# Optimization experiments

Measured on AMD Instinct MI355X. Metric: run time of the kernel, lower is better.

The kernel has to match this reference:

```python
import jax, jax.numpy as jnp
import numpy as np

B, L, D, H, NB = 8, 256, 128, 4, 2
HD = D // H
N_ITEMS, TIME_SPAN = 50000, 256
EPS = 1e-8
NEG = -(2.0 ** 32) + 1.0  # torch uses -2**32+1 padding value


def _ln(x, g, b):
    m = jnp.mean(x, -1, keepdims=True)
    v = jnp.mean((x - m) ** 2, -1, keepdims=True)
    return (x - m) / jnp.sqrt(v + EPS) * g + b


def setup_inputs() -> dict:
    ks = iter(jax.random.split(jax.random.key(0), 40))

    def nrm(shape, s=0.02):
        return jax.random.normal(next(ks), shape, jnp.float32) * s

    inp = {
        "user_ids": jax.random.randint(next(ks), (B,), 0, 1000),
        "log_seqs": jax.random.randint(next(ks), (B, L), 0, N_ITEMS + 1),
        "time_matrices": jax.random.randint(next(ks), (B, L, L), 0, TIME_SPAN + 1),
        "pos_seqs": jax.random.randint(next(ks), (B, L), 1, N_ITEMS + 1),
        "neg_seqs": jax.random.randint(next(ks), (B, L), 1, N_ITEMS + 1),
    }
    inp["item_emb"] = nrm((N_ITEMS + 1, D)).at[0].set(0.0)  # padding_idx=0
    inp["posK_emb"] = nrm((L, D))
    inp["posV_emb"] = nrm((L, D))
    inp["timeK_emb"] = nrm((TIME_SPAN + 1, D))
    inp["timeV_emb"] = nrm((TIME_SPAN + 1, D))
    inp["ln1_g"] = jnp.ones((NB, D)); inp["ln1_b"] = jnp.zeros((NB, D))
    inp["Wq"] = nrm((NB, D, D)); inp["bq"] = jnp.zeros((NB, D))
    inp["Wk"] = nrm((NB, D, D)); inp["bk"] = jnp.zeros((NB, D))
    inp["Wv"] = nrm((NB, D, D)); inp["bv"] = jnp.zeros((NB, D))
    inp["ln2_g"] = jnp.ones((NB, D)); inp["ln2_b"] = jnp.zeros((NB, D))
    inp["W1"] = nrm((NB, D, D)); inp["b1"] = jnp.zeros((NB, D))
    inp["W2"] = nrm((NB, D, D)); inp["b2"] = jnp.zeros((NB, D))
    inp["lnf_g"] = jnp.ones((D,)); inp["lnf_b"] = jnp.zeros((D,))
    return inp


def reference(user_ids, log_seqs, time_matrices, pos_seqs, neg_seqs,
              item_emb, posK_emb, posV_emb, timeK_emb, timeV_emb,
              ln1_g, ln1_b, Wq, bq, Wk, bk, Wv, bv, ln2_g, ln2_b,
              W1, b1, W2, b2, lnf_g, lnf_b):
    # dropout layers are identity in eval mode
    seqs = item_emb[log_seqs] * jnp.sqrt(jnp.float32(D))          # [B,L,D]
    tK = timeK_emb[time_matrices].reshape(B, L, L, H, HD)          # [B,Lq,Lk,H,hd]
    tV = timeV_emb[time_matrices].reshape(B, L, L, H, HD)
    pad = log_seqs == 0                                            # [B,L]
    seqs = seqs * (~pad)[..., None]
    causal = jnp.triu(jnp.ones((L, L), bool), 1)                   # ~tril -> masked
    # time_mask masks by QUERY position (matches torch unsqueeze(-1).expand)
    mask = pad[:, None, :, None] | causal[None, None]              # [B,1,Lq,Lk]
    posKh = posK_emb.reshape(L, H, HD)
    posVh = posV_emb.reshape(L, H, HD)
    for i in range(NB):
        q_in = _ln(seqs, ln1_g[i], ln1_b[i])
        Qh = (q_in @ Wq[i] + bq[i]).reshape(B, L, H, HD).transpose(0, 2, 1, 3)
        Kh = (seqs @ Wk[i] + bk[i]).reshape(B, L, H, HD).transpose(0, 2, 1, 3)
        Vh = (seqs @ Wv[i] + bv[i]).reshape(B, L, H, HD).transpose(0, 2, 1, 3)
        scores = jnp.einsum("bhqd,bhkd->bhqk", Qh, Kh)
        scores = scores + jnp.einsum("bhqd,khd->bhqk", Qh, posKh)
        scores = scores + jnp.einsum("bqkhd,bhqd->bhqk", tK, Qh)
        scores = scores / jnp.sqrt(jnp.float32(HD))
        scores = jnp.where(mask, NEG, scores)
        A = jax.nn.softmax(scores, axis=-1)                        # [B,H,Lq,Lk]
        out = jnp.einsum("bhqk,bhkd->bhqd", A, Vh)
        out = out + jnp.einsum("bhqk,khd->bhqd", A, posVh)
        out = out + jnp.einsum("bhqk,bqkhd->bhqd", A, tV)
        out = out.transpose(0, 2, 1, 3).reshape(B, L, D)
        seqs = q_in + out                                          # residual on Q
        seqs = _ln(seqs, ln2_g[i], ln2_b[i])
        h = jax.nn.relu(seqs @ W1[i] + b1[i])                      # conv1d k=1 == linear
        seqs = seqs + (h @ W2[i] + b2[i])
        seqs = seqs * (~pad)[..., None]
    feats = _ln(seqs, lnf_g, lnf_b)
    pos_logits = jnp.sum(feats * item_emb[pos_seqs], -1)           # [B,L]
    neg_logits = jnp.sum(feats * item_emb[neg_seqs], -1)
    return (pos_logits, neg_logits)
```

## Files before the change

kernel.cpp:

```cpp
#include <hip/hip_runtime.h>
#include <hip/hip_bf16.h>

#define L_ 256
#define H_ 4
#define ROWS 2048
#define NEGV (-4294967295.0f)

typedef unsigned short us16;

__device__ __forceinline__ float us2f(us16 u){ return __uint_as_float(((unsigned)u)<<16); }
__device__ __forceinline__ us16 f2us(float f){ __hip_bfloat16 h=__float2bfloat16(f); return *(us16*)&h; }

struct KArgs {
    const int *log_seqs, *tmat, *pos_seqs, *neg_seqs;
    const float *item_emb, *posK, *posV, *timeK, *timeV;
    const float *ln1g, *ln1b, *bq, *bk, *bv, *ln2g, *ln2b, *b1, *b2, *lnfg, *lnfb;
    const float *Wq, *Wk, *Wv, *W1, *W2;
    float *qin0, *qin1, *out;
    us16 *wsW, *tmK, *tmV, *Qb0, *Kb0, *Vb0, *Qb1, *Kb1, *Vb1;
};

__device__ __forceinline__ void stage_w(const us16* __restrict__ Wg, us16* sW, int tid){
    const uint4* src=(const uint4*)Wg;
    uint4* dst=(uint4*)sW;
    #pragma unroll
    for(int j=0;j<8;j++) dst[j*256+tid]=src[j*256+tid];
}

__device__ __forceinline__ void ln_rows(float* sA,
        const float* __restrict__ g, const float* __restrict__ b,
        float* qin_out, int r0, int tid){
    int r=tid>>5, l=tid&31;
    float* x=sA+r*128;
    float x0=x[l],x1=x[l+32],x2=x[l+64],x3=x[l+96];
    float s=x0+x1+x2+x3;
    #pragma unroll
    for(int o=16;o;o>>=1) s+=__shfl_xor(s,o,64);
    float m=s*(1.f/128.f);
    float d0=x0-m,d1=x1-m,d2=x2-m,d3=x3-m;
    float v=d0*d0+d1*d1+d2*d2+d3*d3;
    #pragma unroll
    for(int o=16;o;o>>=1) v+=__shfl_xor(v,o,64);
    float rstd=rsqrtf(v*(1.f/128.f)+1e-8f);
    float y0=d0*rstd*g[l]+b[l];
    float y1=d1*rstd*g[l+32]+b[l+32];
    float y2=d2*rstd*g[l+64]+b[l+64];
    float y3=d3*rstd*g[l+96]+b[l+96];
    x[l]=y0; x[l+32]=y1; x[l+64]=y2; x[l+96]=y3;
    if(qin_out){
        float* q=qin_out+(size_t)(r0+r)*128;
        q[l]=y0; q[l+32]=y1; q[l+64]=y2; q[l+96]=y3;
    }
}

__device__ __forceinline__ void gemm2x2(const float* A, const us16* sW,
        int ra, int rb, int c0, float* acc){
    float a00=0,a01=0,a10=0,a11=0;
    const float* Ar=A+ra*128;
    const float* Br=A+rb*128;
    #pragma unroll 8
    for(int k=0;k<128;k++){
        ushort2 wp=*(const ushort2*)(sW+k*128+c0);
        float w0=us2f(wp.x), w1=us2f(wp.y);
        float x0=Ar[k], x1=Br[k];
        a00=fmaf(x0,w0,a00); a01=fmaf(x0,w1,a01);
        a10=fmaf(x1,w0,a10); a11=fmaf(x1,w1,a11);
    }
    acc[0]=a00; acc[1]=a01; acc[2]=a10; acc[3]=a11;
}

__global__ __launch_bounds__(256) void k_pre(KArgs a){
    __shared__ __align__(16) char smem[36864];
    int tid=threadIdx.x, bid=blockIdx.x;
    if(bid<768){
        us16* sW=(us16*)smem;
        float* sA=(float*)(smem+32768);
        int m=bid>>8, rg=bid&255, r0=rg*8;
        {
            int rl=tid>>5, c4=tid&31;
            int id=a.log_seqs[r0+rl];
            float4 v=((const float4*)a.item_emb)[id*32+c4];
            float sc = id? 11.3137085f : 0.f;
            v.x*=sc; v.y*=sc; v.z*=sc; v.w*=sc;
            ((float4*)sA)[tid]=v;
        }
        const float* Wsrc=(m==0)?a.Wq:(m==1)?a.Wk:a.Wv;
        {
            const float4* src=(const float4*)Wsrc;
            ushort4* dst=(ushort4*)sW;
            #pragma unroll
            for(int j=0;j<16;j++){
                float4 w=src[j*256+tid];
                ushort4 o; o.x=f2us(w.x);o.y=f2us(w.y);o.z=f2us(w.z);o.w=f2us(w.w);
                dst[j*256+tid]=o;
            }
        }
        __syncthreads();
        if(m==0){ ln_rows(sA, a.ln1g, a.ln1b, a.qin0, r0, tid); __syncthreads(); }
        int cp=tid&63, rp=tid>>6, c0=2*cp, ra=2*rp, rb=ra+1;
        float acc[4];
        gemm2x2(sA,sW,ra,rb,c0,acc);
        if(m==0){
            float b0v=a.bq[c0], b1v=a.bq[c0+1];
            ushort2 s0; s0.x=f2us(acc[0]+b0v); s0.y=f2us(acc[1]+b1v);
            ushort2 s1; s1.x=f2us(acc[2]+b0v); s1.y=f2us(acc[3]+b1v);
            *(ushort2*)(a.Qb0+(size_t)(r0+ra)*128+c0)=s0;
            *(ushort2*)(a.Qb0+(size_t)(r0+rb)*128+c0)=s1;
        } else {
            const float* bb=(m==1)?a.bk:a.bv;
            const float* pp=(m==1)?a.posK:a.posV;
            us16* Oo=(m==1)?a.Kb0:a.Vb0;
            int qa=(r0+ra)&255, qb2=(r0+rb)&255;
            float b0v=bb[c0], b1v=bb[c0+1];
            ushort2 s0; s0.x=f2us(acc[0]+b0v+pp[qa*128+c0]);  s0.y=f2us(acc[1]+b1v+pp[qa*128+c0+1]);
            ushort2 s1; s1.x=f2us(acc[2]+b0v+pp[qb2*128+c0]); s1.y=f2us(acc[3]+b1v+pp[qb2*128+c0+1]);
            *(ushort2*)(Oo+(size_t)(r0+ra)*128+c0)=s0;
            *(ushort2*)(Oo+(size_t)(r0+rb)*128+c0)=s1;
        }
    } else if(bid<880){
        int j=bid-768; int m=j>>4; int idx=(j&15)*256+tid;
        const float* base;
        switch(m){
            case 0: base=a.W1; break;        case 1: base=a.W2; break;
            case 2: base=a.Wq+16384; break;  case 3: base=a.Wk+16384; break;
            case 4: base=a.Wv+16384; break;  case 5: base=a.W1+16384; break;
            default: base=a.W2+16384; break;
        }
        float4 v=((const float4*)base)[idx];
        ushort4 o; o.x=f2us(v.x);o.y=f2us(v.y);o.z=f2us(v.z);o.w=f2us(v.w);
        ((ushort4*)(a.wsW+(size_t)m*16384))[idx]=o;
    } else {
        int gi=(bid-880)*256+tid;
        if(gi<8224){
            float4 v=((const float4*)a.timeK)[gi];
            ushort4 o; o.x=f2us(v.x);o.y=f2us(v.y);o.z=f2us(v.z);o.w=f2us(v.w);
            ((ushort4*)a.tmK)[gi]=o;
        } else if(gi<16448){
            int g2=gi-8224;
            float4 v=((const float4*)a.timeV)[g2];
            ushort4 o; o.x=f2us(v.x);o.y=f2us(v.y);o.z=f2us(v.z);o.w=f2us(v.w);
            ((ushort4*)a.tmV)[g2]=o;
        }
    }
}

__global__ __launch_bounds__(256,4) void k_blk(KArgs a, int layer){
    __shared__ __align__(16) char smem[36864];
    float* sQ  =(float*)smem;
    float* sS  =(float*)(smem+1024);
    int*   sTM =(int*)  (smem+9216);
    float* sPr =(float*)(smem+11264);
    float* sRed=(float*)(smem+19456);
    float* sRed2=(float*)(smem+19472);
    us16*  sW  =(us16*) smem;
    float* sX  =(float*)(smem+32768);
    float* sH  =(float*)(smem+33792);
    float* sY  =(float*)(smem+34816);
    float* sRB =(float*)(smem+35840);

    int tid=threadIdx.x, bid=blockIdx.x;
    int b=bid>>7, p=bid&127;
    int q1=p, q2=255-p, b0=b*L_;
    int r1=b0+q1, r2=b0+q2;
    bool pad1=a.log_seqs[r1]==0, pad2=a.log_seqs[r2]==0;
    const us16* Qb = layer? a.Qb1:a.Qb0;
    const us16* Kb = layer? a.Kb1:a.Kb0;
    const us16* Vb = layer? a.Vb1:a.Vb0;
    const float* qin = layer? a.qin1:a.qin0;
    const float scale=0.17677669529663687f;
    if(tid<128) sQ[tid]=us2f(Qb[(size_t)r1*128+tid])*scale;
    else        sQ[tid]=us2f(Qb[(size_t)r2*128+(tid-128)])*scale;
    int k=tid;
    int tm1=a.tmat[(size_t)r1*L_+k], tm2=a.tmat[(size_t)r2*L_+k];
    sTM[k]=tm1; sTM[256+k]=tm2;
    __syncthreads();

    {
        const uint4* K4=(const uint4*)(Kb+(size_t)(b0+k)*128);
        #pragma unroll
        for(int i2=0;i2<2;i2++){
            int qq=i2?q2:q1; bool pad=i2?pad2:pad1;
            int tm=i2?tm2:tm1;
            bool act=(k<=qq)&&!pad;
            float acc[4]={0.f,0.f,0.f,0.f};
            if(act){
                const uint4* T4=(const uint4*)(a.tmK+(size_t)tm*128);
                const float4* Q4=(const float4*)(sQ+i2*128);
                #pragma unroll
                for(int c=0;c<16;c++){
                    uint4 kv=K4[c]; uint4 tv=T4[c];
                    float4 qa=Q4[2*c], qb=Q4[2*c+1];
                    const us16* ku=(const us16*)&kv;
                    const us16* tu=(const us16*)&tv;
                    acc[c>>2]+= qa.x*(us2f(ku[0])+us2f(tu[0]))
                              + qa.y*(us2f(ku[1])+us2f(tu[1]))
                              + qa.z*(us2f(ku[2])+us2f(tu[2]))
                              + qa.w*(us2f(ku[3])+us2f(tu[3]))
                              + qb.x*(us2f(ku[4])+us2f(tu[4]))
                              + qb.y*(us2f(ku[5])+us2f(tu[5]))
                              + qb.z*(us2f(ku[6])+us2f(tu[6]))
                              + qb.w*(us2f(ku[7])+us2f(tu[7]));
                }
            }
            #pragma unroll
            for(int h=0;h<H_;h++) sS[(i2*4+h)*256+k]= act? acc[h]:NEGV;
        }
    }
    __syncthreads();

    {
        int h=tid>>6, lane=tid&63;
        #pragma unroll
        for(int i2=0;i2<2;i2++){
            float* row=sS+(i2*4+h)*256;
            float v0=row[lane],v1=row[lane+64],v2=row[lane+128],v3=row[lane+192];
            float mm=fmaxf(fmaxf(v0,v1),fmaxf(v2,v3));
            #pragma unroll
            for(int o=32;o;o>>=1) mm=fmaxf(mm,__shfl_xor(mm,o,64));
            float e0=__expf(v0-mm),e1=__expf(v1-mm),e2=__expf(v2-mm),e3=__expf(v3-mm);
            float ss=e0+e1+e2+e3;
            #pragma unroll
            for(int o=32;o;o>>=1) ss+=__shfl_xor(ss,o,64);
            float inv=1.f/ss;
            row[lane]=e0*inv; row[lane+64]=e1*inv; row[lane+128]=e2*inv; row[lane+192]=e3*inv;
        }
    }
    __syncthreads();

    {
        int i2=tid>>7, s8=(tid>>4)&7, dq=tid&15;
        int qq=i2?q2:q1; bool pad=i2?pad2:pad1;
        int kend=pad?L_:qq+1;
        int k0=s8*32;
        int kmax=kend-k0; kmax=kmax<0?0:(kmax>32?32:kmax);
        const float* row=sS+(i2*4+(dq>>2))*256;
        const int* tmrow=sTM+i2*256;
        float a0=0,a1=0,a2=0,a3=0,a4=0,a5=0,a6=0,a7=0;
        for(int kk=0;kk<kmax;kk++){
            int kx=k0+kk;
            float aa=row[kx];
            int tmk=tmrow[kx];
            uint4 v4=((const uint4*)(Vb+(size_t)(b0+kx)*128))[dq];
            uint4 t4=((const uint4*)(a.tmV+(size_t)tmk*128))[dq];
            const us16* vu=(const us16*)&v4;
            const us16* tu=(const us16*)&t4;
            a0=fmaf(aa,us2f(vu[0])+us2f(tu[0]),a0);
            a1=fmaf(aa,us2f(vu[1])+us2f(tu[1]),a1);
            a2=fmaf(aa,us2f(vu[2])+us2f(tu[2]),a2);
            a3=fmaf(aa,us2f(vu[3])+us2f(tu[3]),a3);
            a4=fmaf(aa,us2f(vu[4])+us2f(tu[4]),a4);
            a5=fmaf(aa,us2f(vu[5])+us2f(tu[5]),a5);
            a6=fmaf(aa,us2f(vu[6])+us2f(tu[6]),a6);
            a7=fmaf(aa,us2f(vu[7])+us2f(tu[7]),a7);
        }
        float* dst=sPr+(i2*8+s8)*128+dq*8;
        ((float4*)dst)[0]=make_float4(a0,a1,a2,a3);
        ((float4*)dst)[1]=make_float4(a4,a5,a6,a7);
    }
    __syncthreads();

    int ii=tid>>7, l=tid&127;
    bool padown = ii? pad2:pad1;
    int rr = ii? r2:r1;
    int qown = ii? q2:q1;
    {
        float v=qin[(size_t)rr*128+l];
        #pragma unroll
        for(int sl=0;sl<8;sl++) v+=sPr[(ii*8+sl)*128+l];
        float s=v;
        #pragma unroll
        for(int o=32;o;o>>=1) s+=__shfl_xor(s,o,64);
        if((tid&63)==0) sRed[ii*2+((tid>>6)&1)]=s;
        __syncthreads();
        float m=(sRed[ii*2]+sRed[ii*2+1])*(1.f/128.f);
        float d=v-m;
        float vv=d*d;
        #pragma unroll
        for(int o=32;o;o>>=1) vv+=__shfl_xor(vv,o,64);
        if((tid&63)==0) sRed2[ii*2+((tid>>6)&1)]=vv;
        __syncthreads();
        float rstd=rsqrtf((sRed2[ii*2]+sRed2[ii*2+1])*(1.f/128.f)+1e-8f);
        float y=d*rstd*a.ln2g[layer*128+l]+a.ln2b[layer*128+l];
        __syncthreads();
        sX[ii*128+l]=y;
    }
    __syncthreads();

    int cc=l;
    stage_w(a.wsW+(size_t)(layer?5:0)*16384, sW, tid);
    __syncthreads();
    {
        const float* xr=sX+ii*128;
        float h=0;
        #pragma unroll 16
        for(int k2=0;k2<128;k2++) h=fmaf(xr[k2],us2f(sW[k2*128+cc]),h);
        h=fmaxf(h+a.b1[layer*128+cc],0.f);
        __syncthreads();
        sH[ii*128+cc]=h;
    }
    __syncthreads();
    stage_w(a.wsW+(size_t)(layer?6:1)*16384, sW, tid);
    __syncthreads();
    float f;
    {
        const float* hr=sH+ii*128;
        float acc=0;
        #pragma unroll 16
        for(int k2=0;k2<128;k2++) acc=fmaf(hr[k2],us2f(sW[k2*128+cc]),acc);
        f=acc+a.b2[layer*128+cc]+sX[ii*128+cc];
        if(padown) f=0.f;
    }
    __syncthreads();

    if(layer==0){
        sY[ii*128+cc]=f;
        float s=f;
        #pragma unroll
        for(int o=32;o;o>>=1) s+=__shfl_xor(s,o,64);
        if((tid&63)==0) sRB[ii*2+((tid>>6)&1)]=s;
        __syncthreads();
        float m=(sRB[ii*2]+sRB[ii*2+1])*(1.f/128.f);
        float d=f-m;
        float vv=d*d;
        #pragma unroll
        for(int o=32;o;o>>=1) vv+=__shfl_xor(vv,o,64);
        if((tid&63)==0) sRB[4+ii*2+((tid>>6)&1)]=vv;
        __syncthreads();
        float rstd=rsqrtf((sRB[4+ii*2]+sRB[5+ii*2])*(1.f/128.f)+1e-8f);
        float y1=d*rstd*a.ln1g[128+cc]+a.ln1b[128+cc];
        a.qin1[(size_t)rr*128+cc]=y1;
        sX[ii*128+cc]=y1;
        __syncthreads();
        stage_w(a.wsW+(size_t)2*16384, sW, tid);
        __syncthreads();
        {
            const float* xr=sX+ii*128;
            float acc=0;
            #pragma unroll 16
            for(int k2=0;k2<128;k2++) acc=fmaf(xr[k2],us2f(sW[k2*128+cc]),acc);
            acc+=a.bq[128+cc];
            a.Qb1[(size_t)rr*128+cc]=f2us(acc);
        }
        __syncthreads();
        stage_w(a.wsW+(size_t)3*16384, sW, tid);
        __syncthreads();
        {
            const float* yr=sY+ii*128;
            float acc=0;
            #pragma unroll 16
            for(int k2=0;k2<128;k2++) acc=fmaf(yr[k2],us2f(sW[k2*128+cc]),acc);
            acc+=a.bk[128+cc]+a.posK[qown*128+cc];
            a.Kb1[(size_t)rr*128+cc]=f2us(acc);
        }
        __syncthreads();
        stage_w(a.wsW+(size_t)4*16384, sW, tid);
        __syncthreads();
        {
            const float* yr=sY+ii*128;
            float acc=0;
            #pragma unroll 16
            for(int k2=0;k2<128;k2++) acc=fmaf(yr[k2],us2f(sW[k2*128+cc]),acc);
            acc+=a.bv[128+cc]+a.posV[qown*128+cc];
            a.Vb1[(size_t)rr*128+cc]=f2us(acc);
        }
    } else {
        float s=f;
        #pragma unroll
        for(int o=32;o;o>>=1) s+=__shfl_xor(s,o,64);
        if((tid&63)==0) sRB[ii*2+((tid>>6)&1)]=s;
        __syncthreads();
        float m=(sRB[ii*2]+sRB[ii*2+1])*(1.f/128.f);
        float d=f-m;
        float vv=d*d;
        #pragma unroll
        for(int o=32;o;o>>=1) vv+=__shfl_xor(vv,o,64);
        if((tid&63)==0) sRB[4+ii*2+((tid>>6)&1)]=vv;
        __syncthreads();
        float rstd=rsqrtf((sRB[4+ii*2]+sRB[5+ii*2])*(1.f/128.f)+1e-8f);
        sX[ii*128+cc]=d*rstd*a.lnfg[cc]+a.lnfb[cc];
        __syncthreads();
        int w=tid>>6, lane=tid&63;
        int rowi=w>>1, neg=w&1;
        int rg = rowi? r2:r1;
        int id = neg? a.neg_seqs[rg] : a.pos_seqs[rg];
        const float* e=a.item_emb+(size_t)id*128;
        float s2 = sX[rowi*128+lane]*e[lane] + sX[rowi*128+lane+64]*e[lane+64];
        #pragma unroll
        for(int o=32;o;o>>=1) s2+=__shfl_xor(s2,o,64);
        if(lane==0) a.out[neg*ROWS+rg]=s2;
    }
}

extern "C" void kernel_launch(void* const* d_in, const int* in_sizes, int n_in,
                              void* d_out, int out_size, void* d_ws, size_t ws_size,
                              hipStream_t stream) {
    KArgs a;
    a.log_seqs=(const int*)d_in[1];
    a.tmat    =(const int*)d_in[2];
    a.pos_seqs=(const int*)d_in[3];
    a.neg_seqs=(const int*)d_in[4];
    a.item_emb=(const float*)d_in[5];
    a.posK =(const float*)d_in[6];
    a.posV =(const float*)d_in[7];
    a.timeK=(const float*)d_in[8];
    a.timeV=(const float*)d_in[9];
    a.ln1g=(const float*)d_in[10];
    a.ln1b=(const float*)d_in[11];
    a.Wq=(const float*)d_in[12];
    a.bq=(const float*)d_in[13];
    a.Wk=(const float*)d_in[14];
    a.bk=(const float*)d_in[15];
    a.Wv=(const float*)d_in[16];
    a.bv=(const float*)d_in[17];
    a.ln2g=(const float*)d_in[18];
    a.ln2b=(const float*)d_in[19];
    a.W1=(const float*)d_in[20];
    a.b1=(const float*)d_in[21];
    a.W2=(const float*)d_in[22];
    a.b2=(const float*)d_in[23];
    a.lnfg=(const float*)d_in[24];
    a.lnfb=(const float*)d_in[25];

    const size_t MB=1u<<20;
    char* w=(char*)d_ws;
    a.qin0=(float*)(w+0*MB);
    a.qin1=(float*)(w+1*MB);
    a.Qb0 =(us16*) (w+2*MB);
    a.Kb0 =(us16*) (w+2*MB+512*1024);
    a.Vb0 =(us16*) (w+3*MB);
    a.Qb1 =(us16*) (w+3*MB+512*1024);
    a.Kb1 =(us16*) (w+4*MB);
    a.Vb1 =(us16*) (w+4*MB+512*1024);
    a.wsW =(us16*) (w+5*MB);
    a.tmK =(us16*) (w+5*MB+256*1024);
    a.tmV =(us16*) (w+5*MB+384*1024);
    a.out =(float*)d_out;

    k_pre<<<946,256,0,stream>>>(a);
    k_blk<<<1024,256,0,stream>>>(a,0);
    k_blk<<<1024,256,0,stream>>>(a,1);
}
```

Before: 213.2 us.

## Use bf16 dot2 with k-pair-packed weights and V, drop LDS weight staging

Weights are pre-packed as bf16 pairs interleaved along k, and V is stored with row pairs interleaved, so the score, PV and small GEMV loops can use the v_dot2 bf16 instruction instead of scalar unpack-and-FMA. The per-block LDS staging of weight matrices and its barriers are removed; the GEMVs now read packed weights straight from global/L2, and k_pre reads fp32 weights directly. Softmax probabilities and activations are kept in bf16 in LDS, which shrinks shared memory and may raise occupancy. The cost is reduced precision in the probabilities and activations, plus uncoalesced global weight reads in place of shared-memory reads.

```diff
diff --git a/kernel.cpp b/kernel.cpp
--- a/kernel.cpp
+++ b/kernel.cpp
@@ -10,6 +10,18 @@
 
 __device__ __forceinline__ float us2f(us16 u){ return __uint_as_float(((unsigned)u)<<16); }
 __device__ __forceinline__ us16 f2us(float f){ __hip_bfloat16 h=__float2bfloat16(f); return *(us16*)&h; }
+
+__device__ __forceinline__ float dot2bf(unsigned x, unsigned y, float c){
+#if __has_builtin(__builtin_amdgcn_fdot2_f32_bf16)
+    typedef __bf16 bf2 __attribute__((ext_vector_type(2)));
+    union U{ unsigned u; bf2 v; };
+    U ux, uy; ux.u=x; uy.u=y;
+    return __builtin_amdgcn_fdot2_f32_bf16(ux.v, uy.v, c, false);
+#else
+    float r=fmaf(us2f((us16)(x&0xffffu)), us2f((us16)(y&0xffffu)), c);
+    return fmaf(us2f((us16)(x>>16)), us2f((us16)(y>>16)), r);
+#endif
+}
 
 struct KArgs {
     const int *log_seqs, *tmat, *pos_seqs, *neg_seqs;
@@ -17,15 +29,9 @@
     const float *ln1g, *ln1b, *bq, *bk, *bv, *ln2g, *ln2b, *b1, *b2, *lnfg, *lnfb;
     const float *Wq, *Wk, *Wv, *W1, *W2;
     float *qin0, *qin1, *out;
-    us16 *wsW, *tmK, *tmV, *Qb0, *Kb0, *Vb0, *Qb1, *Kb1, *Vb1;
+    unsigned *wsP;
+    us16 *tmK, *tmV, *Qb0, *Kb0, *Vb0, *Qb1, *Kb1, *Vb1;
 };
-
-__device__ __forceinline__ void stage_w(const us16* __restrict__ Wg, us16* sW, int tid){
-    const uint4* src=(const uint4*)Wg;
-    uint4* dst=(uint4*)sW;
-    #pragma unroll
-    for(int j=0;j<8;j++) dst[j*256+tid]=src[j*256+tid];
-}
 
 __device__ __forceinline__ void ln_rows(float* sA,
         const float* __restrict__ g, const float* __restrict__ b,
@@ -53,28 +59,21 @@
     }
 }
 
-__device__ __forceinline__ void gemm2x2(const float* A, const us16* sW,
-        int ra, int rb, int c0, float* acc){
-    float a00=0,a01=0,a10=0,a11=0;
-    const float* Ar=A+ra*128;
-    const float* Br=A+rb*128;
+__device__ __forceinline__ float gemv128(const unsigned* __restrict__ wp,
+                                         const unsigned* __restrict__ xp, int c){
+    float s0=0.f, s1=0.f;
     #pragma unroll 8
-    for(int k=0;k<128;k++){
-        ushort2 wp=*(const ushort2*)(sW+k*128+c0);
-        float w0=us2f(wp.x), w1=us2f(wp.y);
-        float x0=Ar[k], x1=Br[k];
-        a00=fmaf(x0,w0,a00); a01=fmaf(x0,w1,a01);
-        a10=fmaf(x1,w0,a10); a11=fmaf(x1,w1,a11);
-    }
-    acc[0]=a00; acc[1]=a01; acc[2]=a10; acc[3]=a11;
+    for(int kp=0;kp<64;kp+=2){
+        s0=dot2bf(xp[kp],   wp[kp*128+c],     s0);
+        s1=dot2bf(xp[kp+1], wp[(kp+1)*128+c], s1);
+    }
+    return s0+s1;
 }
 
 __global__ __launch_bounds__(256) void k_pre(KArgs a){
-    __shared__ __align__(16) char smem[36864];
+    __shared__ __align__(16) float sA[1024];
     int tid=threadIdx.x, bid=blockIdx.x;
     if(bid<768){
-        us16* sW=(us16*)smem;
-        float* sA=(float*)(smem+32768);
         int m=bid>>8, rg=bid&255, r0=rg*8;
         {
             int rl=tid>>5, c4=tid&31;
@@ -84,41 +83,47 @@
             v.x*=sc; v.y*=sc; v.z*=sc; v.w*=sc;
             ((float4*)sA)[tid]=v;
         }
+        __syncthreads();
+        if(m==0){ ln_rows(sA, a.ln1g, a.ln1b, a.qin0, r0, tid); __syncthreads(); }
         const float* Wsrc=(m==0)?a.Wq:(m==1)?a.Wk:a.Wv;
-        {
-            const float4* src=(const float4*)Wsrc;
-            ushort4* dst=(ushort4*)sW;
-            #pragma unroll
-            for(int j=0;j<16;j++){
-                float4 w=src[j*256+tid];
-                ushort4 o; o.x=f2us(w.x);o.y=f2us(w.y);o.z=f2us(w.z);o.w=f2us(w.w);
-                dst[j*256+tid]=o;
-            }
-        }
-        __syncthreads();
-        if(m==0){ ln_rows(sA, a.ln1g, a.ln1b, a.qin0, r0, tid); __syncthreads(); }
         int cp=tid&63, rp=tid>>6, c0=2*cp, ra=2*rp, rb=ra+1;
-        float acc[4];
-        gemm2x2(sA,sW,ra,rb,c0,acc);
+        float a00=0,a01=0,a10=0,a11=0;
+        const float* Ar=sA+ra*128;
+        const float* Br=sA+rb*128;
+        #pragma unroll 8
+        for(int kk=0;kk<128;kk++){
+            float2 wp=((const float2*)(Wsrc+(size_t)kk*128))[cp];
+            float x0=Ar[kk], x1=Br[kk];
+            a00=fmaf(x0,wp.x,a00); a01=fmaf(x0,wp.y,a01);
+            a10=fmaf(x1,wp.x,a10); a11=fmaf(x1,wp.y,a11);
+        }
+        int r_a=r0+ra, r_b=r0+rb;
         if(m==0){
             float b0v=a.bq[c0], b1v=a.bq[c0+1];
-            ushort2 s0; s0.x=f2us(acc[0]+b0v); s0.y=f2us(acc[1]+b1v);
-            ushort2 s1; s1.x=f2us(acc[2]+b0v); s1.y=f2us(acc[3]+b1v);
-            *(ushort2*)(a.Qb0+(size_t)(r0+ra)*128+c0)=s0;
-            *(ushort2*)(a.Qb0+(size_t)(r0+rb)*128+c0)=s1;
+            ushort2 s0; s0.x=f2us(a00+b0v); s0.y=f2us(a01+b1v);
+            ushort2 s1; s1.x=f2us(a10+b0v); s1.y=f2us(a11+b1v);
+            *(ushort2*)(a.Qb0+(size_t)r_a*128+c0)=s0;
+            *(ushort2*)(a.Qb0+(size_t)r_b*128+c0)=s1;
+        } else if(m==1){
+            float b0v=a.bk[c0], b1v=a.bk[c0+1];
+            int qa=r_a&255, qb2=r_b&255;
+            ushort2 s0; s0.x=f2us(a00+b0v+a.posK[qa*128+c0]);  s0.y=f2us(a01+b1v+a.posK[qa*128+c0+1]);
+            ushort2 s1; s1.x=f2us(a10+b0v+a.posK[qb2*128+c0]); s1.y=f2us(a11+b1v+a.posK[qb2*128+c0+1]);
+            *(ushort2*)(a.Kb0+(size_t)r_a*128+c0)=s0;
+            *(ushort2*)(a.Kb0+(size_t)r_b*128+c0)=s1;
         } else {
-            const float* bb=(m==1)?a.bk:a.bv;
-            const float* pp=(m==1)?a.posK:a.posV;
-            us16* Oo=(m==1)?a.Kb0:a.Vb0;
-            int qa=(r0+ra)&255, qb2=(r0+rb)&255;
-            float b0v=bb[c0], b1v=bb[c0+1];
-            ushort2 s0; s0.x=f2us(acc[0]+b0v+pp[qa*128+c0]);  s0.y=f2us(acc[1]+b1v+pp[qa*128+c0+1]);
-            ushort2 s1; s1.x=f2us(acc[2]+b0v+pp[qb2*128+c0]); s1.y=f2us(acc[3]+b1v+pp[qb2*128+c0+1]);
-            *(ushort2*)(Oo+(size_t)(r0+ra)*128+c0)=s0;
-            *(ushort2*)(Oo+(size_t)(r0+rb)*128+c0)=s1;
+            float b0v=a.bv[c0], b1v=a.bv[c0+1];
+            int qa=r_a&255, qb2=r_b&255;
+            unsigned lo0=f2us(a00+b0v+a.posV[qa*128+c0]);
+            unsigned lo1=f2us(a01+b1v+a.posV[qa*128+c0+1]);
+            unsigned hi0=f2us(a10+b0v+a.posV[qb2*128+c0]);
+            unsigned hi1=f2us(a11+b1v+a.posV[qb2*128+c0+1]);
+            unsigned* Vo=(unsigned*)a.Vb0+((size_t)r_a>>1)*128;
+            Vo[c0]  =lo0|(hi0<<16);
+            Vo[c0+1]=lo1|(hi1<<16);
         }
     } else if(bid<880){
-        int j=bid-768; int m=j>>4; int idx=(j&15)*256+tid;
+        int j=bid-768; int m=j>>4; int sub=j&15;
         const float* base;
         switch(m){
             case 0: base=a.W1; break;        case 1: base=a.W2; break;
@@ -126,9 +131,15 @@
             case 4: base=a.Wv+16384; break;  case 5: base=a.W1+16384; break;
             default: base=a.W2+16384; break;
         }
-        float4 v=((const float4*)base)[idx];
-        ushort4 o; o.x=f2us(v.x);o.y=f2us(v.y);o.z=f2us(v.z);o.w=f2us(v.w);
-        ((ushort4*)(a.wsW+(size_t)m*16384))[idx]=o;
+        unsigned* dst=a.wsP+(size_t)m*8192;
+        #pragma unroll
+        for(int t2=0;t2<2;t2++){
+            int o=sub*512+t2*256+tid;
+            int kp=o>>7, c=o&127;
+            unsigned lo=f2us(base[(size_t)(2*kp)*128+c]);
+            unsigned hi=f2us(base[(size_t)(2*kp+1)*128+c]);
+            dst[o]=lo|(hi<<16);
+        }
     } else {
         int gi=(bid-880)*256+tid;
         if(gi<8224){
@@ -145,18 +156,16 @@
 }
 
 __global__ __launch_bounds__(256,4) void k_blk(KArgs a, int layer){
-    __shared__ __align__(16) char smem[36864];
-    float* sQ  =(float*)smem;
-    float* sS  =(float*)(smem+1024);
-    int*   sTM =(int*)  (smem+9216);
-    float* sPr =(float*)(smem+11264);
-    float* sRed=(float*)(smem+19456);
-    float* sRed2=(float*)(smem+19472);
-    us16*  sW  =(us16*) smem;
-    float* sX  =(float*)(smem+32768);
-    float* sH  =(float*)(smem+33792);
-    float* sY  =(float*)(smem+34816);
-    float* sRB =(float*)(smem+35840);
+    __shared__ __align__(16) float    sS[8*256];
+    __shared__ __align__(16) unsigned sAb[8*128];
+    __shared__ __align__(16) unsigned sQb[128];
+    __shared__ __align__(16) int      sTM[512];
+    __shared__ __align__(16) float    sPr[16*128];
+    __shared__ float sRed[4], sRed2[4], sRB[8];
+    __shared__ __align__(16) float    sX[256];
+    __shared__ __align__(16) unsigned sXb[128];
+    __shared__ __align__(16) unsigned sHb[128];
+    __shared__ __align__(16) unsigned sYb[128];
 
     int tid=threadIdx.x, bid=blockIdx.x;
     int b=bid>>7, p=bid&127;
@@ -165,11 +174,15 @@
     bool pad1=a.log_seqs[r1]==0, pad2=a.log_seqs[r2]==0;
     const us16* Qb = layer? a.Qb1:a.Qb0;
     const us16* Kb = layer? a.Kb1:a.Kb0;
-    const us16* Vb = layer? a.Vb1:a.Vb0;
+    const unsigned* Vbu = (const unsigned*)(layer? a.Vb1:a.Vb0);
     const float* qin = layer? a.qin1:a.qin0;
     const float scale=0.17677669529663687f;
-    if(tid<128) sQ[tid]=us2f(Qb[(size_t)r1*128+tid])*scale;
-    else        sQ[tid]=us2f(Qb[(size_t)r2*128+(tid-128)])*scale;
+
+    if(tid<128){
+        int rowq=tid>>6, j=tid&63;
+        int r=rowq?r2:r1;
+        sQb[rowq*64+j]=((const unsigned*)Qb)[(size_t)r*64+j];
+    }
     int k=tid;
     int tm1=a.tmat[(size_t)r1*L_+k], tm2=a.tmat[(size_t)r2*L_+k];
     sTM[k]=tm1; sTM[256+k]=tm2;
@@ -185,34 +198,30 @@
             float acc[4]={0.f,0.f,0.f,0.f};
             if(act){
                 const uint4* T4=(const uint4*)(a.tmK+(size_t)tm*128);
-                const float4* Q4=(const float4*)(sQ+i2*128);
+                const uint4* Q4=(const uint4*)(sQb+i2*64);
                 #pragma unroll
                 for(int c=0;c<16;c++){
-                    uint4 kv=K4[c]; uint4 tv=T4[c];
-                    float4 qa=Q4[2*c], qb=Q4[2*c+1];
-                    const us16* ku=(const us16*)&kv;
-                    const us16* tu=(const us16*)&tv;
-                    acc[c>>2]+= qa.x*(us2f(ku[0])+us2f(tu[0]))
-                              + qa.y*(us2f(ku[1])+us2f(tu[1]))
-                              + qa.z*(us2f(ku[2])+us2f(tu[2]))
-                              + qa.w*(us2f(ku[3])+us2f(tu[3]))
-                              + qb.x*(us2f(ku[4])+us2f(tu[4]))
-                              + qb.y*(us2f(ku[5])+us2f(tu[5]))
-                              + qb.z*(us2f(ku[6])+us2f(tu[6]))
-                              + qb.w*(us2f(ku[7])+us2f(tu[7]));
+                    uint4 kv=K4[c], tv=T4[c], qv=Q4[c];
+                    float t=acc[c>>2];
+                    t=dot2bf(qv.x,kv.x,t); t=dot2bf(qv.y,kv.y,t);
+                    t=dot2bf(qv.z,kv.z,t); t=dot2bf(qv.w,kv.w,t);
+                    t=dot2bf(qv.x,tv.x,t); t=dot2bf(qv.y,tv.y,t);
+                    t=dot2bf(qv.z,tv.z,t); t=dot2bf(qv.w,tv.w,t);
+                    acc[c>>2]=t;
                 }
             }
             #pragma unroll
-            for(int h=0;h<H_;h++) sS[(i2*4+h)*256+k]= act? acc[h]:NEGV;
+            for(int h2=0;h2<H_;h2++) sS[(i2*4+h2)*256+k]= act? acc[h2]*scale : NEGV;
         }
     }
     __syncthreads();
 
     {
         int h=tid>>6, lane=tid&63;
+        us16* sab=(us16*)sAb;
         #pragma unroll
         for(int i2=0;i2<2;i2++){
-            float* row=sS+(i2*4+h)*256;
+            const float* row=sS+(i2*4+h)*256;
             float v0=row[lane],v1=row[lane+64],v2=row[lane+128],v3=row[lane+192];
             float mm=fmaxf(fmaxf(v0,v1),fmaxf(v2,v3));
             #pragma unroll
@@ -222,7 +231,9 @@
             #pragma unroll
             for(int o=32;o;o>>=1) ss+=__shfl_xor(ss,o,64);
             float inv=1.f/ss;
-            row[lane]=e0*inv; row[lane+64]=e1*inv; row[lane+128]=e2*inv; row[lane+192]=e3*inv;
+            us16* ar=sab+(i2*4+h)*256;
+            ar[lane]    =f2us(e0*inv); ar[lane+64] =f2us(e1*inv);
+            ar[lane+128]=f2us(e2*inv); ar[lane+192]=f2us(e3*inv);
         }
     }
     __syncthreads();
@@ -233,29 +244,38 @@
         int kend=pad?L_:qq+1;
         int k0=s8*32;
         int kmax=kend-k0; kmax=kmax<0?0:(kmax>32?32:kmax);
-        const float* row=sS+(i2*4+(dq>>2))*256;
+        int npair=(kmax+1)>>1;
+        const unsigned* arow=sAb+(i2*4+(dq>>2))*128;
         const int* tmrow=sTM+i2*256;
-        float a0=0,a1=0,a2=0,a3=0,a4=0,a5=0,a6=0,a7=0;
-        for(int kk=0;kk<kmax;kk++){
-            int kx=k0+kk;
-            float aa=row[kx];
-            int tmk=tmrow[kx];
-            uint4 v4=((const uint4*)(Vb+(size_t)(b0+kx)*128))[dq];
-            uint4 t4=((const uint4*)(a.tmV+(size_t)tmk*128))[dq];
-            const us16* vu=(const us16*)&v4;
-            const us16* tu=(const us16*)&t4;
-            a0=fmaf(aa,us2f(vu[0])+us2f(tu[0]),a0);
-            a1=fmaf(aa,us2f(vu[1])+us2f(tu[1]),a1);
-            a2=fmaf(aa,us2f(vu[2])+us2f(tu[2]),a2);
-            a3=fmaf(aa,us2f(vu[3])+us2f(tu[3]),a3);
-            a4=fmaf(aa,us2f(vu[4])+us2f(tu[4]),a4);
-            a5=fmaf(aa,us2f(vu[5])+us2f(tu[5]),a5);
-            a6=fmaf(aa,us2f(vu[6])+us2f(tu[6]),a6);
-            a7=fmaf(aa,us2f(vu[7])+us2f(tu[7]),a7);
+        float ac0=0,ac1=0,ac2=0,ac3=0,ac4=0,ac5=0,ac6=0,ac7=0;
+        for(int kp=0;kp<npair;kp++){
+            int kx=k0+2*kp;
+            unsigned aa=arow[kx>>1];
+            int tma=tmrow[kx], tmb=tmrow[kx+1];
+            const uint4* Vp=(const uint4*)(Vbu+((size_t)(b0+kx)>>1)*128+dq*8);
+            uint4 va=Vp[0], vb4=Vp[1];
+            uint4 ta=((const uint4*)(a.tmV+(size_t)tma*128))[dq];
+            uint4 tb=((const uint4*)(a.tmV+(size_t)tmb*128))[dq];
+            ac0=dot2bf(aa,va.x,ac0);  ac1=dot2bf(aa,va.y,ac1);
+            ac2=dot2bf(aa,va.z,ac2);  ac3=dot2bf(aa,va.w,ac3);
+            ac4=dot2bf(aa,vb4.x,ac4); ac5=dot2bf(aa,vb4.y,ac5);
+            ac6=dot2bf(aa,vb4.z,ac6); ac7=dot2bf(aa,vb4.w,ac7);
+            unsigned p0=__builtin_amdgcn_perm(tb.x,ta.x,0x05040100u);
+            unsigned p1=__builtin_amdgcn_perm(tb.x,ta.x,0x07060302u);
+            unsigned p2=__builtin_amdgcn_perm(tb.y,ta.y,0x05040100u);
+            unsigned p3=__builtin_amdgcn_perm(tb.y,ta.y,0x07060302u);
+            unsigned p4=__builtin_amdgcn_perm(tb.z,ta.z,0x05040100u);
+            unsigned p5=__builtin_amdgcn_perm(tb.z,ta.z,0x07060302u);
+            unsigned p6=__builtin_amdgcn_perm(tb.w,ta.w,0x05040100u);
+            unsigned p7=__builtin_amdgcn_perm(tb.w,ta.w,0x07060302u);
+            ac0=dot2bf(aa,p0,ac0); ac1=dot2bf(aa,p1,ac1);
+            ac2=dot2bf(aa,p2,ac2); ac3=dot2bf(aa,p3,ac3);
+            ac4=dot2bf(aa,p4,ac4); ac5=dot2bf(aa,p5,ac5);
+            ac6=dot2bf(aa,p6,ac6); ac7=dot2bf(aa,p7,ac7);
         }
         float* dst=sPr+(i2*8+s8)*128+dq*8;
-        ((float4*)dst)[0]=make_float4(a0,a1,a2,a3);
-        ((float4*)dst)[1]=make_float4(a4,a5,a6,a7);
+        ((float4*)dst)[0]=make_float4(ac0,ac1,ac2,ac3);
+        ((float4*)dst)[1]=make_float4(ac4,ac5,ac6,ac7);
     }
     __syncthreads();
 
@@ -281,39 +301,28 @@
         __syncthreads();
         float rstd=rsqrtf((sRed2[ii*2]+sRed2[ii*2+1])*(1.f/128.f)+1e-8f);
         float y=d*rstd*a.ln2g[layer*128+l]+a.ln2b[layer*128+l];
-        __syncthreads();
         sX[ii*128+l]=y;
+        ((us16*)sXb)[ii*128+l]=f2us(y);
     }
     __syncthreads();
 
     int cc=l;
-    stage_w(a.wsW+(size_t)(layer?5:0)*16384, sW, tid);
-    __syncthreads();
-    {
-        const float* xr=sX+ii*128;
-        float h=0;
-        #pragma unroll 16
-        for(int k2=0;k2<128;k2++) h=fmaf(xr[k2],us2f(sW[k2*128+cc]),h);
-        h=fmaxf(h+a.b1[layer*128+cc],0.f);
-        __syncthreads();
-        sH[ii*128+cc]=h;
-    }
-    __syncthreads();
-    stage_w(a.wsW+(size_t)(layer?6:1)*16384, sW, tid);
+    {
+        const unsigned* W1p=a.wsP+(size_t)(layer?5:0)*8192;
+        float h1=gemv128(W1p, sXb+ii*64, cc);
+        h1=fmaxf(h1+a.b1[layer*128+cc],0.f);
+        ((us16*)sHb)[ii*128+cc]=f2us(h1);
+    }
     __syncthreads();
     float f;
     {
-        const float* hr=sH+ii*128;
-        float acc=0;
-        #pragma unroll 16
-        for(int k2=0;k2<128;k2++) acc=fmaf(hr[k2],us2f(sW[k2*128+cc]),acc);
-        f=acc+a.b2[layer*128+cc]+sX[ii*128+cc];
+        const unsigned* W2p=a.wsP+(size_t)(layer?6:1)*8192;
+        f=gemv128(W2p, sHb+ii*64, cc)+a.b2[layer*128+cc]+sX[ii*128+cc];
         if(padown) f=0.f;
     }
-    __syncthreads();
 
     if(layer==0){
-        sY[ii*128+cc]=f;
+        ((us16*)sYb)[ii*128+cc]=f2us(f);
         float s=f;
         #pragma unroll
         for(int o=32;o;o>>=1) s+=__shfl_xor(s,o,64);
@@ -329,40 +338,14 @@
         float rstd=rsqrtf((sRB[4+ii*2]+sRB[5+ii*2])*(1.f/128.f)+1e-8f);
         float y1=d*rstd*a.ln1g[128+cc]+a.ln1b[128+cc];
         a.qin1[(size_t)rr*128+cc]=y1;
-        sX[ii*128+cc]=y1;
-        __syncthreads();
-        stage_w(a.wsW+(size_t)2*16384, sW, tid);
-        __syncthreads();
-        {
-            const float* xr=sX+ii*128;
-            float acc=0;
-            #pragma unroll 16
-            for(int k2=0;k2<128;k2++) acc=fmaf(xr[k2],us2f(sW[k2*128+cc]),acc);
-            acc+=a.bq[128+cc];
-            a.Qb1[(size_t)rr*128+cc]=f2us(acc);
-        }
-        __syncthreads();
-        stage_w(a.wsW+(size_t)3*16384, sW, tid);
-        __syncthreads();
-        {
-            const float* yr=sY+ii*128;
-            float acc=0;
-            #pragma unroll 16
-            for(int k2=0;k2<128;k2++) acc=fmaf(yr[k2],us2f(sW[k2*128+cc]),acc);
-            acc+=a.bk[128+cc]+a.posK[qown*128+cc];
-            a.Kb1[(size_t)rr*128+cc]=f2us(acc);
-        }
-        __syncthreads();
-        stage_w(a.wsW+(size_t)4*16384, sW, tid);
-        __syncthreads();
-        {
-            const float* yr=sY+ii*128;
-            float acc=0;
-            #pragma unroll 16
-            for(int k2=0;k2<128;k2++) acc=fmaf(yr[k2],us2f(sW[k2*128+cc]),acc);
-            acc+=a.bv[128+cc]+a.posV[qown*128+cc];
-            a.Vb1[(size_t)rr*128+cc]=f2us(acc);
-        }
+        ((us16*)sXb)[ii*128+cc]=f2us(y1);
+        __syncthreads();
+        float accq=gemv128(a.wsP+(size_t)2*8192, sXb+ii*64, cc)+a.bq[128+cc];
+        a.Qb1[(size_t)rr*128+cc]=f2us(accq);
+        float acck=gemv128(a.wsP+(size_t)3*8192, sYb+ii*64, cc)+a.bk[128+cc]+a.posK[qown*128+cc];
+        a.Kb1[(size_t)rr*128+cc]=f2us(acck);
+        float accv=gemv128(a.wsP+(size_t)4*8192, sYb+ii*64, cc)+a.bv[128+cc]+a.posV[qown*128+cc];
+        ((us16*)a.Vb1)[((size_t)rr>>1)*256+2*cc+(rr&1)]=f2us(accv);
     } else {
         float s=f;
         #pragma unroll
@@ -431,7 +414,7 @@
     a.Qb1 =(us16*) (w+3*MB+512*1024);
     a.Kb1 =(us16*) (w+4*MB);
     a.Vb1 =(us16*) (w+4*MB+512*1024);
-    a.wsW =(us16*) (w+5*MB);
+    a.wsP =(unsigned*)(w+5*MB);
     a.tmK =(us16*) (w+5*MB+256*1024);
     a.tmV =(us16*) (w+5*MB+384*1024);
     a.out =(float*)d_out;
```

Measured after the change: 203.0 us. 1.05x faster.
